# Kernel tuning notes

Measured on AMD Instinct MI355X. Metric: run time of the kernel, lower is better.

## Reference

```python
import jax, jax.numpy as jnp
import numpy as np

QUERY_DIM = 1024
KV_DIM = 768
NUM_HEADS = 16
HEAD_DIM = QUERY_DIM // NUM_HEADS


def setup_inputs() -> dict:
    key = jax.random.key(0)
    ks = jax.random.split(key, 11)
    B, Sq, Skv = 4, 2048, 2048
    s_q = 1.0 / np.sqrt(QUERY_DIM)
    s_kv = 1.0 / np.sqrt(KV_DIM)
    return {
        "query": jax.random.normal(ks[0], (B, Sq, QUERY_DIM), jnp.float32),
        "key": jax.random.normal(ks[1], (B, Skv, KV_DIM), jnp.float32),
        "value": jax.random.normal(ks[2], (B, Skv, KV_DIM), jnp.float32),
        "Wq": jax.random.uniform(ks[3], (QUERY_DIM, QUERY_DIM), jnp.float32, -s_q, s_q),
        "bq": jax.random.uniform(ks[4], (QUERY_DIM,), jnp.float32, -s_q, s_q),
        "Wk": jax.random.uniform(ks[5], (KV_DIM, QUERY_DIM), jnp.float32, -s_kv, s_kv),
        "bk": jax.random.uniform(ks[6], (QUERY_DIM,), jnp.float32, -s_kv, s_kv),
        "Wv": jax.random.uniform(ks[7], (KV_DIM, QUERY_DIM), jnp.float32, -s_kv, s_kv),
        "bv": jax.random.uniform(ks[8], (QUERY_DIM,), jnp.float32, -s_kv, s_kv),
        "Wo": jax.random.uniform(ks[9], (QUERY_DIM, QUERY_DIM), jnp.float32, -s_q, s_q),
        "bo": jax.random.uniform(ks[10], (QUERY_DIM,), jnp.float32, -s_q, s_q),
    }


def reference(query, key, value, Wq, bq, Wk, bk, Wv, bv, Wo, bo):
    B, Sq, _ = query.shape
    Skv = key.shape[1]
    H, D = NUM_HEADS, HEAD_DIM
    # linear projections, then split heads: [B, H, S, D]
    q = (query @ Wq + bq).reshape(B, Sq, H, D).transpose(0, 2, 1, 3)
    k = (key @ Wk + bk).reshape(B, Skv, H, D).transpose(0, 2, 1, 3)
    v = (value @ Wv + bv).reshape(B, Skv, H, D).transpose(0, 2, 1, 3)
    scores = jnp.einsum("bhqd,bhkd->bhqk", q, k) / np.sqrt(D).astype(jnp.float32)
    probs = jax.nn.softmax(scores, axis=-1)
    ctx = jnp.einsum("bhqk,bhkd->bhqd", probs, v)
    ctx = ctx.transpose(0, 2, 1, 3).reshape(B, Sq, H * D)
    return ctx @ Wo + bo
```

## Files before the change

kernel.cpp:

```cpp
#include <hip/hip_runtime.h>

typedef unsigned short u16;
typedef unsigned int u32;
typedef unsigned long long u64;
typedef __attribute__((ext_vector_type(8))) short bf16x8;
typedef __attribute__((ext_vector_type(4))) float f32x4;

__device__ __forceinline__ u16 f2bf(float f) {
  union { float f; u32 u; } v; v.f = f;
  u32 r = v.u + 0x7fffu + ((v.u >> 16) & 1u);
  return (u16)(r >> 16);
}
__device__ __forceinline__ u32 pack2bf(float a, float b) {
  union { float f; u32 u; } x, y; x.f = a; y.f = b;
  return ((y.u + 0x8000u) & 0xffff0000u) | ((x.u + 0x8000u) >> 16);
}

__device__ __forceinline__ void gll16(const u16* g, u16* l) {
  __builtin_amdgcn_global_load_lds((__attribute__((address_space(1))) void*)(void*)g,
                                   (__attribute__((address_space(3))) void*)(void*)l,
                                   16, 0, 0);
}

__global__ void conv_bf16(const float* __restrict__ in, u16* __restrict__ out, int n) {
  int i = (blockIdx.x * 256 + threadIdx.x) * 4;
  if (i < n) {
    float4 v = *(const float4*)(in + i);
    ushort4 o;
    o.x = f2bf(v.x); o.y = f2bf(v.y); o.z = f2bf(v.z); o.w = f2bf(v.w);
    *(ushort4*)(out + i) = o;
  }
}

__global__ void transpose_bf16(const float* __restrict__ W, u16* __restrict__ T,
                               int K, int N) {
  __shared__ u16 tile[64 * 72];
  const int k0 = blockIdx.x * 64, n0 = blockIdx.y * 64;
  const int t = threadIdx.x, c = t & 63, rb = t >> 6;
#pragma unroll
  for (int rr = 0; rr < 64; rr += 4) {
    int r = rr + rb;
    tile[r * 72 + c] = f2bf(W[(size_t)(k0 + r) * N + n0 + c]);
  }
  __syncthreads();
#pragma unroll
  for (int rr = 0; rr < 64; rr += 4) {
    int n = rr + rb;
    T[(size_t)(n0 + n) * K + k0 + c] = tile[c * 72 + n];
  }
}

__global__ __launch_bounds__(256, 3) void gemm_bf16(
    const u16* __restrict__ A, const u16* __restrict__ Bt,
    const float* __restrict__ bias, u16* __restrict__ outb,
    float* __restrict__ outf, int K, int mode) {
  __shared__ __align__(16) u16 smem[18432];
  u16* lA = smem;
  u16* lB = smem + 128 * 64;
  const int tid = threadIdx.x;
  const int bm = blockIdx.x * 128;
  const int bn = blockIdx.y * 128;
  const int wid = tid >> 6, lane = tid & 63;
  const int wm = (wid >> 1) * 64, wn = (wid & 1) * 64;
  const int lrow = lane & 15, quad = lane >> 4;
  const int wrow = lane >> 3, wchk = lane & 7;
  const int sw = lrow & 7;
  f32x4 acc[4][4] = {};
  for (int k0 = 0; k0 < K; k0 += 64) {
    const u16* gA = A + (size_t)(bm + wid * 32) * K + k0;
    const u16* gB = Bt + (size_t)(bn + wid * 32) * K + k0;
#pragma unroll
    for (int c = 0; c < 4; c++) {
      gll16(gA + (size_t)(c * 8 + wrow) * K + (wchk ^ wrow) * 8, &lA[(wid * 32 + c * 8) * 64]);
      gll16(gB + (size_t)(c * 8 + wrow) * K + (wchk ^ wrow) * 8, &lB[(wid * 32 + c * 8) * 64]);
    }
    __syncthreads();
#pragma unroll
    for (int ks = 0; ks < 2; ks++) {
      bf16x8 af[4], bfr[4];
#pragma unroll
      for (int i = 0; i < 4; i++)
        af[i] = *(const bf16x8*)&lA[(wm + i * 16 + lrow) * 64 + ((ks * 4 + quad) ^ sw) * 8];
#pragma unroll
      for (int j = 0; j < 4; j++)
        bfr[j] = *(const bf16x8*)&lB[(wn + j * 16 + lrow) * 64 + ((ks * 4 + quad) ^ sw) * 8];
#pragma unroll
      for (int i = 0; i < 4; i++)
#pragma unroll
        for (int j = 0; j < 4; j++)
          acc[i][j] = __builtin_amdgcn_mfma_f32_16x16x32_bf16(af[i], bfr[j], acc[i][j], 0, 0, 0);
    }
    __syncthreads();
  }
  if (mode == 1) {
    u16* tile = smem + wid * (64 * 72);
#pragma unroll
    for (int i = 0; i < 4; i++)
#pragma unroll
      for (int j = 0; j < 4; j++)
#pragma unroll
        for (int r = 0; r < 4; r++) {
          int s_l = i * 16 + quad * 4 + r;
          int d_l = j * 16 + lrow;
          tile[d_l * 72 + s_l] = f2bf(acc[i][j][r] + bias[bn + wn + d_l]);
        }
    __syncthreads();
#pragma unroll
    for (int dd = 0; dd < 8; dd++) {
      int d_l = dd * 8 + (lane >> 3);
      int s_l = (lane & 7) * 8;
      bf16x8 vv = *(const bf16x8*)&tile[d_l * 72 + s_l];
      int row = bm + wm + s_l;
      int col = bn + wn + d_l;
      int b = row >> 11, s = row & 2047;
      int h = col >> 6, d = col & 63;
      *(bf16x8*)&outb[((size_t)(b * 16 + h) * 64 + d) * 2048 + s] = vv;
    }
    return;
  }
#pragma unroll
  for (int i = 0; i < 4; i++)
#pragma unroll
    for (int j = 0; j < 4; j++)
#pragma unroll
      for (int r = 0; r < 4; r++) {
        int row = bm + wm + i * 16 + quad * 4 + r;
        int col = bn + wn + j * 16 + lrow;
        float v = acc[i][j][r] + bias[col];
        if (mode == 2) {
          outf[(size_t)row * 1024 + col] = v;
        } else {
          int b = row >> 11, s = row & 2047;
          int h = col >> 6, d = col & 63;
          outb[((size_t)(b * 16 + h) * 2048 + s) * 64 + d] = f2bf(v);
        }
      }
}

__global__ __launch_bounds__(256, 3) void flash_attn(
    const u16* __restrict__ Q, const u16* __restrict__ Kt,
    const u16* __restrict__ Vt, u16* __restrict__ ctx) {
  __shared__ __align__(16) u16 smem[26624];
  u16* lK = smem;
  u16* lV = smem + 8192;
  const int tid = threadIdx.x, wid = tid >> 6, lane = tid & 63;
  u16* lP = smem + 16384 + wid * 2560;
  const int bh = blockIdx.x;
  const int q0 = blockIdx.y * 64;
  const int lrow = lane & 15, quad = lane >> 4;
  const int sw = lrow & 7;
  const size_t base = (size_t)bh * 2048 * 64;
  bf16x8 qf[4][2];
#pragma unroll
  for (int qt = 0; qt < 4; qt++)
#pragma unroll
    for (int ks = 0; ks < 2; ks++)
      qf[qt][ks] = *(const bf16x8*)(Q + base + (size_t)(q0 + qt * 16 + lrow) * 64 + ks * 32 + quad * 8);
  f32x4 of[4][4] = {};
  float lsumq[4] = {0.f, 0.f, 0.f, 0.f};
  const int wrow8 = lane >> 3, wchk8 = lane & 7;
  const int wrow16 = lane >> 4, wchk16 = lane & 15;
  const float C = 0.18033688011112042f;
  for (int kv0 = 0; kv0 < 2048; kv0 += 128) {
    __syncthreads();
    const u16* gK = Kt + base + (size_t)(kv0 + wid * 32) * 64;
    const u16* gV = Vt + base + (size_t)(wid * 16) * 2048 + kv0;
#pragma unroll
    for (int c = 0; c < 4; c++) {
      gll16(gK + (size_t)(c * 8 + wrow8) * 64 + (wchk8 ^ wrow8) * 8,
            &lK[(wid * 32 + c * 8) * 64]);
      gll16(gV + (size_t)(c * 4 + wrow16) * 2048 + (wchk16 ^ (c * 4 + wrow16)) * 8,
            &lV[(wid * 16 + c * 4) * 128]);
    }
    __syncthreads();
    f32x4 sfT[2][4];
#pragma unroll
    for (int nt = 0; nt < 2; nt++) {
      bf16x8 kf0 = *(const bf16x8*)&lK[((wid * 2 + nt) * 16 + lrow) * 64 + (quad ^ sw) * 8];
      bf16x8 kf1 = *(const bf16x8*)&lK[((wid * 2 + nt) * 16 + lrow) * 64 + ((4 + quad) ^ sw) * 8];
#pragma unroll
      for (int qt = 0; qt < 4; qt++) {
        f32x4 s = {};
        s = __builtin_amdgcn_mfma_f32_16x16x32_bf16(kf0, qf[qt][0], s, 0, 0, 0);
        s = __builtin_amdgcn_mfma_f32_16x16x32_bf16(kf1, qf[qt][1], s, 0, 0, 0);
        sfT[nt][qt] = s;
      }
    }
#pragma unroll
    for (int nt = 0; nt < 2; nt++)
#pragma unroll
      for (int qt = 0; qt < 4; qt++) {
        float p0 = __builtin_amdgcn_exp2f(sfT[nt][qt][0] * C);
        float p1 = __builtin_amdgcn_exp2f(sfT[nt][qt][1] * C);
        float p2 = __builtin_amdgcn_exp2f(sfT[nt][qt][2] * C);
        float p3 = __builtin_amdgcn_exp2f(sfT[nt][qt][3] * C);
        lsumq[qt] += (p0 + p1) + (p2 + p3);
        u64 pk = ((u64)pack2bf(p2, p3) << 32) | pack2bf(p0, p1);
        *(u64*)&lP[(qt * 16 + lrow) * 40 + nt * 16 + quad * 4] = pk;
      }
    __asm__ volatile("s_waitcnt lgkmcnt(0)" ::: "memory");
#pragma unroll
    for (int qt = 0; qt < 4; qt++) {
      bf16x8 pf = *(const bf16x8*)&lP[(qt * 16 + lrow) * 40 + quad * 8];
#pragma unroll
      for (int dt = 0; dt < 4; dt++) {
        bf16x8 vf = *(const bf16x8*)&lV[(dt * 16 + lrow) * 128 + ((wid * 4 + quad) ^ lrow) * 8];
        of[qt][dt] = __builtin_amdgcn_mfma_f32_16x16x32_bf16(pf, vf, of[qt][dt], 0, 0, 0);
      }
    }
  }
  float lsw[4];
#pragma unroll
  for (int qt = 0; qt < 4; qt++) {
    float v = lsumq[qt];
    v += __shfl_xor(v, 16, 64);
    v += __shfl_xor(v, 32, 64);
    lsw[qt] = v;
  }
  __syncthreads();
  float* lsums = (float*)(smem + 16384);
  if (quad == 0) {
#pragma unroll
    for (int qt = 0; qt < 4; qt++) lsums[wid * 64 + qt * 16 + lrow] = lsw[qt];
  }
  float* rbuf = (float*)smem;
  for (int w = 0; w < 4; w++) {
    if (wid == w) {
#pragma unroll
      for (int qt = 0; qt < 4; qt++)
#pragma unroll
        for (int dt = 0; dt < 4; dt++)
#pragma unroll
          for (int r = 0; r < 4; r++) {
            int q = qt * 16 + quad * 4 + r;
            int d = dt * 16 + lrow;
            if (w == 0) rbuf[q * 66 + d] = of[qt][dt][r];
            else        rbuf[q * 66 + d] += of[qt][dt][r];
          }
    }
    __syncthreads();
  }
  const int b = bh >> 4, h = bh & 15;
#pragma unroll
  for (int it = 0; it < 2; it++) {
    int q = wid * 16 + it * 8 + (lane >> 3);
    int d0 = (lane & 7) * 8;
    float inv = 1.f / (lsums[q] + lsums[64 + q] + lsums[128 + q] + lsums[192 + q]);
    u16 o[8];
#pragma unroll
    for (int j = 0; j < 8; j++) o[j] = f2bf(rbuf[q * 66 + d0 + j] * inv);
    *(bf16x8*)&ctx[((size_t)b * 2048 + q0 + q) * 1024 + h * 64 + d0] = *(bf16x8*)o;
  }
}

extern "C" void kernel_launch(void* const* d_in, const int* in_sizes, int n_in,
                              void* d_out, int out_size, void* d_ws, size_t ws_size,
                              hipStream_t stream) {
  const float* query = (const float*)d_in[0];
  const float* key   = (const float*)d_in[1];
  const float* value = (const float*)d_in[2];
  const float* Wq = (const float*)d_in[3];
  const float* bq = (const float*)d_in[4];
  const float* Wk = (const float*)d_in[5];
  const float* bk = (const float*)d_in[6];
  const float* Wv = (const float*)d_in[7];
  const float* bv = (const float*)d_in[8];
  const float* Wo = (const float*)d_in[9];
  const float* bo = (const float*)d_in[10];
  float* out = (float*)d_out;
  char* ws = (char*)d_ws;

  const size_t SZ_QKV = (size_t)8192 * 1024 * 2;
  const size_t SZ_KIN = (size_t)8192 * 768 * 2;
  u16* q_ws  = (u16*)(ws);
  u16* k_ws  = (u16*)(ws + SZ_QKV);
  u16* vt_ws = (u16*)(ws + 2 * SZ_QKV);
  u16* qin   = (u16*)(ws + 3 * SZ_QKV);
  u16* kin   = (u16*)(ws + 4 * SZ_QKV);
  u16* vin   = (u16*)(ws + 4 * SZ_QKV + SZ_KIN);
  u16* ctx   = qin;
  u16* wq_t  = (u16*)(ws + 4 * SZ_QKV + 2 * SZ_KIN);
  u16* wk_t  = wq_t + 1024 * 1024;
  u16* wv_t  = wk_t + 1024 * 768;
  u16* wo_t  = wv_t + 1024 * 768;

  conv_bf16<<<8192, 256, 0, stream>>>(query, qin, 8388608);
  conv_bf16<<<6144, 256, 0, stream>>>(key, kin, 6291456);
  conv_bf16<<<6144, 256, 0, stream>>>(value, vin, 6291456);
  transpose_bf16<<<dim3(16, 16), 256, 0, stream>>>(Wq, wq_t, 1024, 1024);
  transpose_bf16<<<dim3(12, 16), 256, 0, stream>>>(Wk, wk_t, 768, 1024);
  transpose_bf16<<<dim3(12, 16), 256, 0, stream>>>(Wv, wv_t, 768, 1024);
  transpose_bf16<<<dim3(16, 16), 256, 0, stream>>>(Wo, wo_t, 1024, 1024);

  gemm_bf16<<<dim3(64, 8), 256, 0, stream>>>(qin, wq_t, bq, q_ws, nullptr, 1024, 0);
  gemm_bf16<<<dim3(64, 8), 256, 0, stream>>>(kin, wk_t, bk, k_ws, nullptr, 768, 0);
  gemm_bf16<<<dim3(64, 8), 256, 0, stream>>>(vin, wv_t, bv, vt_ws, nullptr, 768, 1);

  flash_attn<<<dim3(64, 32), 256, 0, stream>>>(q_ws, k_ws, vt_ws, ctx);

  gemm_bf16<<<dim3(64, 8), 256, 0, stream>>>(ctx, wo_t, bo, nullptr, out, 1024, 2);
}
```

Before: 354.9 us.

## Batch QKV GEMMs into one launch, fold softmax scale into Q, drop LDS staging in attention

The three projection GEMMs now run as one launch over a z grid dimension, and the output GEMM gets its own specialised kernel. The softmax scale is folded into Q in the projection epilogue, which removes a multiply per score in attention. Flash attention now loads its K and V fragments straight from global memory into registers instead of staging them through LDS with barriers. This removes two syncs per KV tile and shrinks LDS use, but each wave now issues uncoalesced, non-shared global loads, and launch bounds drop to 2 blocks per CU.

Measured after the change: 386.7 us. 1.09x slower.

```diff
diff --git a/kernel.cpp b/kernel.cpp
--- a/kernel.cpp
+++ b/kernel.cpp
@@ -21,6 +21,8 @@
                                    (__attribute__((address_space(3))) void*)(void*)l,
                                    16, 0, 0);
 }
+
+#define SCALE_C 0.18033688011112042f
 
 __global__ void conv_bf16(const float* __restrict__ in, u16* __restrict__ out, int n) {
   int i = (blockIdx.x * 256 + threadIdx.x) * 4;
@@ -50,10 +52,18 @@
   }
 }
 
-__global__ __launch_bounds__(256, 3) void gemm_bf16(
-    const u16* __restrict__ A, const u16* __restrict__ Bt,
-    const float* __restrict__ bias, u16* __restrict__ outb,
-    float* __restrict__ outf, int K, int mode) {
+__global__ __launch_bounds__(256, 3) void gemm_qkv(
+    const u16* __restrict__ Aq, const u16* __restrict__ Ak, const u16* __restrict__ Av,
+    const u16* __restrict__ Bwq, const u16* __restrict__ Bwk, const u16* __restrict__ Bwv,
+    const float* __restrict__ bq, const float* __restrict__ bk, const float* __restrict__ bv,
+    u16* __restrict__ oq, u16* __restrict__ ok, u16* __restrict__ ov) {
+  const int z = blockIdx.z;
+  const u16* A = (z == 0) ? Aq : (z == 1) ? Ak : Av;
+  const u16* Bt = (z == 0) ? Bwq : (z == 1) ? Bwk : Bwv;
+  const float* bias = (z == 0) ? bq : (z == 1) ? bk : bv;
+  u16* outb = (z == 0) ? oq : (z == 1) ? ok : ov;
+  const int K = (z == 0) ? 1024 : 768;
+  const float scale = (z == 0) ? SCALE_C : 1.0f;
   __shared__ __align__(16) u16 smem[18432];
   u16* lA = smem;
   u16* lB = smem + 128 * 64;
@@ -92,7 +102,7 @@
     }
     __syncthreads();
   }
-  if (mode == 1) {
+  if (z == 2) {
     u16* tile = smem + wid * (64 * 72);
 #pragma unroll
     for (int i = 0; i < 4; i++)
@@ -126,29 +136,75 @@
       for (int r = 0; r < 4; r++) {
         int row = bm + wm + i * 16 + quad * 4 + r;
         int col = bn + wn + j * 16 + lrow;
-        float v = acc[i][j][r] + bias[col];
-        if (mode == 2) {
-          outf[(size_t)row * 1024 + col] = v;
-        } else {
-          int b = row >> 11, s = row & 2047;
-          int h = col >> 6, d = col & 63;
-          outb[((size_t)(b * 16 + h) * 2048 + s) * 64 + d] = f2bf(v);
-        }
+        float v = (acc[i][j][r] + bias[col]) * scale;
+        int b = row >> 11, s = row & 2047;
+        int h = col >> 6, d = col & 63;
+        outb[((size_t)(b * 16 + h) * 2048 + s) * 64 + d] = f2bf(v);
       }
 }
 
-__global__ __launch_bounds__(256, 3) void flash_attn(
+__global__ __launch_bounds__(256, 3) void gemm_out(
+    const u16* __restrict__ A, const u16* __restrict__ Bt,
+    const float* __restrict__ bias, float* __restrict__ outf) {
+  __shared__ __align__(16) u16 smem[16384];
+  u16* lA = smem;
+  u16* lB = smem + 128 * 64;
+  const int tid = threadIdx.x;
+  const int bm = blockIdx.x * 128;
+  const int bn = blockIdx.y * 128;
+  const int wid = tid >> 6, lane = tid & 63;
+  const int wm = (wid >> 1) * 64, wn = (wid & 1) * 64;
+  const int lrow = lane & 15, quad = lane >> 4;
+  const int wrow = lane >> 3, wchk = lane & 7;
+  const int sw = lrow & 7;
+  f32x4 acc[4][4] = {};
+  for (int k0 = 0; k0 < 1024; k0 += 64) {
+    const u16* gA = A + (size_t)(bm + wid * 32) * 1024 + k0;
+    const u16* gB = Bt + (size_t)(bn + wid * 32) * 1024 + k0;
+#pragma unroll
+    for (int c = 0; c < 4; c++) {
+      gll16(gA + (size_t)(c * 8 + wrow) * 1024 + (wchk ^ wrow) * 8, &lA[(wid * 32 + c * 8) * 64]);
+      gll16(gB + (size_t)(c * 8 + wrow) * 1024 + (wchk ^ wrow) * 8, &lB[(wid * 32 + c * 8) * 64]);
+    }
+    __syncthreads();
+#pragma unroll
+    for (int ks = 0; ks < 2; ks++) {
+      bf16x8 af[4], bfr[4];
+#pragma unroll
+      for (int i = 0; i < 4; i++)
+        af[i] = *(const bf16x8*)&lA[(wm + i * 16 + lrow) * 64 + ((ks * 4 + quad) ^ sw) * 8];
+#pragma unroll
+      for (int j = 0; j < 4; j++)
+        bfr[j] = *(const bf16x8*)&lB[(wn + j * 16 + lrow) * 64 + ((ks * 4 + quad) ^ sw) * 8];
+#pragma unroll
+      for (int i = 0; i < 4; i++)
+#pragma unroll
+        for (int j = 0; j < 4; j++)
+          acc[i][j] = __builtin_amdgcn_mfma_f32_16x16x32_bf16(af[i], bfr[j], acc[i][j], 0, 0, 0);
+    }
+    __syncthreads();
+  }
+#pragma unroll
+  for (int i = 0; i < 4; i++)
+#pragma unroll
+    for (int j = 0; j < 4; j++)
+#pragma unroll
+      for (int r = 0; r < 4; r++) {
+        int row = bm + wm + i * 16 + quad * 4 + r;
+        int col = bn + wn + j * 16 + lrow;
+        outf[(size_t)row * 1024 + col] = acc[i][j][r] + bias[col];
+      }
+}
+
+__global__ __launch_bounds__(256, 2) void flash_attn(
     const u16* __restrict__ Q, const u16* __restrict__ Kt,
     const u16* __restrict__ Vt, u16* __restrict__ ctx) {
-  __shared__ __align__(16) u16 smem[26624];
-  u16* lK = smem;
-  u16* lV = smem + 8192;
+  __shared__ __align__(16) u16 smem[10752];
   const int tid = threadIdx.x, wid = tid >> 6, lane = tid & 63;
-  u16* lP = smem + 16384 + wid * 2560;
+  u16* lP = smem + wid * 2560;
   const int bh = blockIdx.x;
   const int q0 = blockIdx.y * 64;
   const int lrow = lane & 15, quad = lane >> 4;
-  const int sw = lrow & 7;
   const size_t base = (size_t)bh * 2048 * 64;
   bf16x8 qf[4][2];
 #pragma unroll
@@ -158,42 +214,35 @@
       qf[qt][ks] = *(const bf16x8*)(Q + base + (size_t)(q0 + qt * 16 + lrow) * 64 + ks * 32 + quad * 8);
   f32x4 of[4][4] = {};
   float lsumq[4] = {0.f, 0.f, 0.f, 0.f};
-  const int wrow8 = lane >> 3, wchk8 = lane & 7;
-  const int wrow16 = lane >> 4, wchk16 = lane & 15;
-  const float C = 0.18033688011112042f;
   for (int kv0 = 0; kv0 < 2048; kv0 += 128) {
-    __syncthreads();
-    const u16* gK = Kt + base + (size_t)(kv0 + wid * 32) * 64;
-    const u16* gV = Vt + base + (size_t)(wid * 16) * 2048 + kv0;
-#pragma unroll
-    for (int c = 0; c < 4; c++) {
-      gll16(gK + (size_t)(c * 8 + wrow8) * 64 + (wchk8 ^ wrow8) * 8,
-            &lK[(wid * 32 + c * 8) * 64]);
-      gll16(gV + (size_t)(c * 4 + wrow16) * 2048 + (wchk16 ^ (c * 4 + wrow16)) * 8,
-            &lV[(wid * 16 + c * 4) * 128]);
-    }
-    __syncthreads();
+    const int kvw = kv0 + wid * 32;
+    bf16x8 kf[2][2], vf[4];
+#pragma unroll
+    for (int nt = 0; nt < 2; nt++)
+#pragma unroll
+      for (int ks = 0; ks < 2; ks++)
+        kf[nt][ks] = *(const bf16x8*)(Kt + base + (size_t)(kvw + nt * 16 + lrow) * 64 + ks * 32 + quad * 8);
+#pragma unroll
+    for (int dt = 0; dt < 4; dt++)
+      vf[dt] = *(const bf16x8*)(Vt + base + (size_t)(dt * 16 + lrow) * 2048 + kvw + quad * 8);
     f32x4 sfT[2][4];
 #pragma unroll
-    for (int nt = 0; nt < 2; nt++) {
-      bf16x8 kf0 = *(const bf16x8*)&lK[((wid * 2 + nt) * 16 + lrow) * 64 + (quad ^ sw) * 8];
-      bf16x8 kf1 = *(const bf16x8*)&lK[((wid * 2 + nt) * 16 + lrow) * 64 + ((4 + quad) ^ sw) * 8];
+    for (int nt = 0; nt < 2; nt++)
 #pragma unroll
       for (int qt = 0; qt < 4; qt++) {
         f32x4 s = {};
-        s = __builtin_amdgcn_mfma_f32_16x16x32_bf16(kf0, qf[qt][0], s, 0, 0, 0);
-        s = __builtin_amdgcn_mfma_f32_16x16x32_bf16(kf1, qf[qt][1], s, 0, 0, 0);
+        s = __builtin_amdgcn_mfma_f32_16x16x32_bf16(kf[nt][0], qf[qt][0], s, 0, 0, 0);
+        s = __builtin_amdgcn_mfma_f32_16x16x32_bf16(kf[nt][1], qf[qt][1], s, 0, 0, 0);
         sfT[nt][qt] = s;
       }
-    }
 #pragma unroll
     for (int nt = 0; nt < 2; nt++)
 #pragma unroll
       for (int qt = 0; qt < 4; qt++) {
-        float p0 = __builtin_amdgcn_exp2f(sfT[nt][qt][0] * C);
-        float p1 = __builtin_amdgcn_exp2f(sfT[nt][qt][1] * C);
-        float p2 = __builtin_amdgcn_exp2f(sfT[nt][qt][2] * C);
-        float p3 = __builtin_amdgcn_exp2f(sfT[nt][qt][3] * C);
+        float p0 = __builtin_amdgcn_exp2f(sfT[nt][qt][0]);
+        float p1 = __builtin_amdgcn_exp2f(sfT[nt][qt][1]);
+        float p2 = __builtin_amdgcn_exp2f(sfT[nt][qt][2]);
+        float p3 = __builtin_amdgcn_exp2f(sfT[nt][qt][3]);
         lsumq[qt] += (p0 + p1) + (p2 + p3);
         u64 pk = ((u64)pack2bf(p2, p3) << 32) | pack2bf(p0, p1);
         *(u64*)&lP[(qt * 16 + lrow) * 40 + nt * 16 + quad * 4] = pk;
@@ -203,10 +252,8 @@
     for (int qt = 0; qt < 4; qt++) {
       bf16x8 pf = *(const bf16x8*)&lP[(qt * 16 + lrow) * 40 + quad * 8];
 #pragma unroll
-      for (int dt = 0; dt < 4; dt++) {
-        bf16x8 vf = *(const bf16x8*)&lV[(dt * 16 + lrow) * 128 + ((wid * 4 + quad) ^ lrow) * 8];
-        of[qt][dt] = __builtin_amdgcn_mfma_f32_16x16x32_bf16(pf, vf, of[qt][dt], 0, 0, 0);
-      }
+      for (int dt = 0; dt < 4; dt++)
+        of[qt][dt] = __builtin_amdgcn_mfma_f32_16x16x32_bf16(pf, vf[dt], of[qt][dt], 0, 0, 0);
     }
   }
   float lsw[4];
@@ -218,7 +265,7 @@
     lsw[qt] = v;
   }
   __syncthreads();
-  float* lsums = (float*)(smem + 16384);
+  float* lsums = (float*)(smem + 10240);
   if (quad == 0) {
 #pragma unroll
     for (int qt = 0; qt < 4; qt++) lsums[wid * 64 + qt * 16 + lrow] = lsw[qt];
@@ -292,11 +339,10 @@
   transpose_bf16<<<dim3(12, 16), 256, 0, stream>>>(Wv, wv_t, 768, 1024);
   transpose_bf16<<<dim3(16, 16), 256, 0, stream>>>(Wo, wo_t, 1024, 1024);
 
-  gemm_bf16<<<dim3(64, 8), 256, 0, stream>>>(qin, wq_t, bq, q_ws, nullptr, 1024, 0);
-  gemm_bf16<<<dim3(64, 8), 256, 0, stream>>>(kin, wk_t, bk, k_ws, nullptr, 768, 0);
-  gemm_bf16<<<dim3(64, 8), 256, 0, stream>>>(vin, wv_t, bv, vt_ws, nullptr, 768, 1);
+  gemm_qkv<<<dim3(64, 8, 3), 256, 0, stream>>>(qin, kin, vin, wq_t, wk_t, wv_t,
+                                               bq, bk, bv, q_ws, k_ws, vt_ws);
 
   flash_attn<<<dim3(64, 32), 256, 0, stream>>>(q_ws, k_ws, vt_ws, ctx);
 
-  gemm_bf16<<<dim3(64, 8), 256, 0, stream>>>(ctx, wo_t, bo, nullptr, out, 1024, 2);
-}
+  gemm_out<<<dim3(64, 8), 256, 0, stream>>>(ctx, wo_t, bo, out);
+}
```
